# Kernel tuning notes

Measured on AMD Instinct MI355X. Metric: run time of the kernel, lower is better.

## Reference

```python
import jax, jax.numpy as jnp
import numpy as np
from jax import lax

B, T, I, H, L = 512, 2048, 16, 40, 3

def setup_inputs() -> dict:
    key = jax.random.key(0)
    ks = jax.random.split(key, 4 * L + 3)
    bound = 1.0 / np.sqrt(H)
    u = lambda k, shp: jax.random.uniform(k, shp, jnp.float32, -bound, bound)
    inp = {"x": jax.random.normal(ks[0], (B, T, I), jnp.float32)}
    for l in range(L):
        in_dim = I if l == 0 else H
        inp[f"w_ih{l}"] = u(ks[1 + 4 * l], (H, in_dim))
        inp[f"w_hh{l}"] = u(ks[2 + 4 * l], (H, H))
        inp[f"b_ih{l}"] = u(ks[3 + 4 * l], (H,))
        inp[f"b_hh{l}"] = u(ks[4 + 4 * l], (H,))
    inp["fc_w"] = u(ks[4 * L + 1], (1, H))
    inp["fc_b"] = u(ks[4 * L + 2], (1,))
    return inp

def _rnn_layer(x_seq, w_ih, w_hh, b_ih, b_hh):
    # Precompute input projection as one big GEMM: [B, T, H]
    xp = jnp.einsum('bti,hi->bth', x_seq, w_ih) + b_ih + b_hh
    h0 = jnp.zeros((x_seq.shape[0], w_hh.shape[0]), x_seq.dtype)
    def step(h, xt):  # xt: [B, H]
        h = jnp.tanh(xt + h @ w_hh.T)
        return h, h
    _, ys = lax.scan(step, h0, jnp.swapaxes(xp, 0, 1))  # [T, B, H]
    return jnp.swapaxes(ys, 0, 1)  # [B, T, H]

def reference(x, w_ih0, w_hh0, b_ih0, b_hh0,
              w_ih1, w_hh1, b_ih1, b_hh1,
              w_ih2, w_hh2, b_ih2, b_hh2, fc_w, fc_b):
    # Multi-layer tanh RNN (eval mode: inter-layer and final dropout are identity)
    h = _rnn_layer(x, w_ih0, w_hh0, b_ih0, b_hh0)
    h = _rnn_layer(h, w_ih1, w_hh1, b_ih1, b_hh1)
    h = _rnn_layer(h, w_ih2, w_hh2, b_ih2, b_hh2)
    last = h[:, -1, :]                     # [B, H]
    out = last @ fc_w.T + fc_b             # [B, 1]
    return out[:, 0]                       # [B]
```

## Files before the change

kernel.cpp:

```cpp
#include <hip/hip_runtime.h>
#include <cstddef>
#include <cstdint>

#define B_ 512
#define T_ 2048
#define I_ 16
#define H_ 40

typedef __fp16 half_t;
typedef half_t h2 __attribute__((ext_vector_type(2)));
typedef float f4 __attribute__((ext_vector_type(4)));

__device__ __forceinline__ float fast_tanh(float x) {
  float e = __builtin_amdgcn_exp2f(x * 2.8853900817779268f);
  return 1.0f - 2.0f * __builtin_amdgcn_rcpf(e + 1.0f);
}

__device__ __forceinline__ float dot2(h2 a, h2 b, float c) {
  return __builtin_amdgcn_fdot2(a, b, c, false);
}

__device__ __forceinline__ h2 cvtpk_v(float lo, float hi) {
  h2 r;
  asm volatile("v_cvt_pkrtz_f16_f32 %0, %1, %2" : "=v"(r) : "v"(lo), "v"(hi));
  return r;
}

#define PIN(v) asm volatile("" : "+v"(v))

#define GLOAD16(R0, R1, R2, R3, P)                                  \
  asm volatile("global_load_dwordx4 %0, %4, off\n\t"                \
               "global_load_dwordx4 %1, %4, off offset:16\n\t"      \
               "global_load_dwordx4 %2, %4, off offset:32\n\t"      \
               "global_load_dwordx4 %3, %4, off offset:48"          \
               : "=&v"(R0), "=&v"(R1), "=&v"(R2), "=&v"(R3)         \
               : "v"(P))

#define WAITX(N)                                                    \
  do {                                                              \
    asm volatile("s_waitcnt vmcnt(" #N ")" ::: "memory");           \
    __builtin_amdgcn_sched_barrier(0);                              \
  } while (0)

#define LOADW(DST, SRC, STR, N2)                                    \
  _Pragma("unroll") for (int k = 0; k < (N2); ++k) {                \
    DST[k][0] = (half_t)SRC[jr * (STR) + 2 * k];                    \
    DST[k][1] = (half_t)SRC[jr * (STR) + 2 * k + 1];                \
    PIN(DST[k]);                                                    \
  }

#define BCAST(NH, PAIRS) do {                                       \
  int nb_ = __builtin_amdgcn_update_dpp(                            \
      0, __builtin_bit_cast(int, (NH)), 0xB1, 0xf, 0xf, false);     \
  h2 pk_ = __builtin_amdgcn_cvt_pkrtz((NH),                         \
      __builtin_bit_cast(float, nb_));                              \
  int pkb_ = __builtin_bit_cast(int, pk_);                          \
  _Pragma("unroll") for (int p = 0; p < H_ / 2; ++p)                \
    PAIRS[p] = __builtin_bit_cast(h2,                               \
        __builtin_amdgcn_readlane(pkb_, 2 * p));                    \
} while (0)

#define HDS(PAIRS, W, A0, A1, A2, A3)                               \
  _Pragma("unroll") for (int p = 0; p < 5; ++p) {                   \
    A0 = dot2(PAIRS[4 * p + 0], (W)[4 * p + 0], A0);                \
    A1 = dot2(PAIRS[4 * p + 1], (W)[4 * p + 1], A1);                \
    A2 = dot2(PAIRS[4 * p + 2], (W)[4 * p + 2], A2);                \
    A3 = dot2(PAIRS[4 * p + 3], (W)[4 * p + 3], A3);                \
  }

#define STEP(XH) do {                                               \
                                             \
  float a0 = bias0, a1 = 0.f, a2 = 0.f, a3 = 0.f;                   \
  a0 = dot2(XH[0], w0i[0], a0); a1 = dot2(XH[1], w0i[1], a1);       \
  a2 = dot2(XH[2], w0i[2], a2); a3 = dot2(XH[3], w0i[3], a3);       \
  a0 = dot2(XH[4], w0i[4], a0); a1 = dot2(XH[5], w0i[5], a1);       \
  a2 = dot2(XH[6], w0i[6], a2); a3 = dot2(XH[7], w0i[7], a3);       \
  HDS(hp0, w0h, a0, a1, a2, a3);                        \
  const float nh0 = fast_tanh((a0 + a1) + (a2 + a3));               \
  BCAST(nh0, hp0);                                                  \
                                             \
  float b0 = bias1, b1 = 0.f, b2 = 0.f, b3 = 0.f;                   \
  HDS(hp0, w1i, b0, b1, b2, b3);                        \
  HDS(hp1, w1h, b0, b1, b2, b3);                        \
  const float nh1 = fast_tanh((b0 + b1) + (b2 + b3));               \
  BCAST(nh1, hp1);                                                  \
                                             \
  float c0 = bias2, c1 = 0.f, c2 = 0.f, c3 = 0.f;                   \
  HDS(hp1, w2i, c0, c1, c2, c3);                        \
  HDS(hp2, w2h, c0, c1, c2, c3);                        \
  nh2v = fast_tanh((c0 + c1) + (c2 + c3));                          \
  BCAST(nh2v, hp2);                                                 \
} while (0)

#define PACKX(XH, R0, R1, R2, R3)                                   \
  do {                                                              \
    XH[0] = cvtpk_v(R0[0], R0[1]); XH[1] = cvtpk_v(R0[2], R0[3]);   \
    XH[2] = cvtpk_v(R1[0], R1[1]); XH[3] = cvtpk_v(R1[2], R1[3]);   \
    XH[4] = cvtpk_v(R2[0], R2[1]); XH[5] = cvtpk_v(R2[2], R2[3]);   \
    XH[6] = cvtpk_v(R3[0], R3[1]); XH[7] = cvtpk_v(R3[2], R3[3]);   \
  } while (0)

__global__ __launch_bounds__(64)
__attribute__((amdgpu_waves_per_eu(1, 1)))
void rnn3_fused(const float* __restrict__ x,
                const float* __restrict__ wih0, const float* __restrict__ whh0,
                const float* __restrict__ bih0, const float* __restrict__ bhh0,
                const float* __restrict__ wih1, const float* __restrict__ whh1,
                const float* __restrict__ b_ih1, const float* __restrict__ bhh1,
                const float* __restrict__ wih2, const float* __restrict__ whh2,
                const float* __restrict__ bih2, const float* __restrict__ bhh2,
                const float* __restrict__ fcw, const float* __restrict__ fcb,
                float* __restrict__ out) {
  const int b = blockIdx.x;
  const int j = threadIdx.x;
  const int jr = (j < H_) ? j : (H_ - 1);

  h2 w0i[I_ / 2], w0h[H_ / 2], w1i[H_ / 2], w1h[H_ / 2], w2i[H_ / 2], w2h[H_ / 2];
  LOADW(w0i, wih0, I_, I_ / 2)
  LOADW(w0h, whh0, H_, H_ / 2)
  LOADW(w1i, wih1, H_, H_ / 2)
  LOADW(w1h, whh1, H_, H_ / 2)
  LOADW(w2i, wih2, H_, H_ / 2)
  LOADW(w2h, whh2, H_, H_ / 2)

  float bias0 = bih0[jr] + bhh0[jr];  PIN(bias0);
  float bias1 = b_ih1[jr] + bhh1[jr]; PIN(bias1);
  float bias2 = bih2[jr] + bhh2[jr];  PIN(bias2);

  h2 hp0[H_ / 2], hp1[H_ / 2], hp2[H_ / 2];
#pragma unroll
  for (int p = 0; p < H_ / 2; ++p) {
    hp0[p] = h2{(half_t)0.f, (half_t)0.f};
    hp1[p] = h2{(half_t)0.f, (half_t)0.f};
    hp2[p] = h2{(half_t)0.f, (half_t)0.f};
  }

  const float* __restrict__ xb = x + (size_t)b * (T_ * I_);

  f4 rA0, rA1, rA2, rA3, rB0, rB1, rB2, rB3;
  GLOAD16(rA0, rA1, rA2, rA3, xb + 0 * I_);
  GLOAD16(rB0, rB1, rB2, rB3, xb + 1 * I_);

  float nh2v = 0.f;
  h2 xh[8];

  for (int t = 0; t < T_; t += 2) {
    WAITX(4);
    PACKX(xh, rA0, rA1, rA2, rA3);
    STEP(xh);
    { const float* pf = xb + (size_t)((t + 2 < T_) ? t + 2 : T_ - 1) * I_;
      GLOAD16(rA0, rA1, rA2, rA3, pf); }
    WAITX(4);
    PACKX(xh, rB0, rB1, rB2, rB3);
    STEP(xh);
    { const float* pf = xb + (size_t)((t + 3 < T_) ? t + 3 : T_ - 1) * I_;
      GLOAD16(rB0, rB1, rB2, rB3, pf); }
  }

  asm volatile("s_waitcnt vmcnt(0)" ::: "memory");
  __builtin_amdgcn_sched_barrier(0);
  PIN(rA0); PIN(rA1); PIN(rA2); PIN(rA3);
  PIN(rB0); PIN(rB1); PIN(rB2); PIN(rB3);

  const float fw = (j < H_) ? fcw[j] : 0.f;
  float v = nh2v * fw;
#pragma unroll
  for (int off = 32; off > 0; off >>= 1) v += __shfl_down(v, off);
  if (j == 0) out[b] = v + fcb[0];
}

extern "C" void kernel_launch(void* const* d_in, const int* in_sizes, int n_in,
                              void* d_out, int out_size, void* d_ws, size_t ws_size,
                              hipStream_t stream) {
  (void)in_sizes; (void)n_in; (void)d_ws; (void)ws_size; (void)out_size;
  const float* x    = (const float*)d_in[0];
  const float* wih0 = (const float*)d_in[1];
  const float* whh0 = (const float*)d_in[2];
  const float* bih0 = (const float*)d_in[3];
  const float* bhh0 = (const float*)d_in[4];
  const float* wih1 = (const float*)d_in[5];
  const float* whh1 = (const float*)d_in[6];
  const float* bih1 = (const float*)d_in[7];
  const float* bhh1 = (const float*)d_in[8];
  const float* wih2 = (const float*)d_in[9];
  const float* whh2 = (const float*)d_in[10];
  const float* bih2 = (const float*)d_in[11];
  const float* bhh2 = (const float*)d_in[12];
  const float* fcw  = (const float*)d_in[13];
  const float* fcb  = (const float*)d_in[14];
  float* out = (float*)d_out;

  hipLaunchKernelGGL(rnn3_fused, dim3(B_), dim3(64), 0, stream,
                     x, wih0, whh0, bih0, bhh0,
                     wih1, whh1, bih1, bhh1,
                     wih2, whh2, bih2, bhh2,
                     fcw, fcb, out);
}
```

Measured before the change: 926.3 us.

## Replace packed fp16 dot2 with scalar FMAs, bpermute broadcast, plain x loads

The packed v_dot2 fp16 accumulations become pairs of scalar fp32 FMAs on converted halves, and the x input skips fp16 packing and is multiplied in fp32. The hidden-state broadcast now uses ds_bpermute in place of readlane. The hand-written inline-asm global loads with explicit vmcnt waits are replaced by ordinary vector loads, leaving scheduling to the compiler. Together these roughly double the VALU instruction count per step and put LDS-path latency on the serial recurrence, and without explicit waits the prefetch overlap may be lost.

```diff
diff --git a/kernel.cpp b/kernel.cpp
--- a/kernel.cpp
+++ b/kernel.cpp
@@ -16,31 +16,14 @@
   return 1.0f - 2.0f * __builtin_amdgcn_rcpf(e + 1.0f);
 }
 
-__device__ __forceinline__ float dot2(h2 a, h2 b, float c) {
-  return __builtin_amdgcn_fdot2(a, b, c, false);
+__device__ __forceinline__ float fmx(half_t a, half_t b, float c) {
+  return __builtin_fmaf((float)a, (float)b, c);
 }
-
-__device__ __forceinline__ h2 cvtpk_v(float lo, float hi) {
-  h2 r;
-  asm volatile("v_cvt_pkrtz_f16_f32 %0, %1, %2" : "=v"(r) : "v"(lo), "v"(hi));
-  return r;
+__device__ __forceinline__ float fmxf(float a, half_t b, float c) {
+  return __builtin_fmaf(a, (float)b, c);
 }
 
 #define PIN(v) asm volatile("" : "+v"(v))
-
-#define GLOAD16(R0, R1, R2, R3, P)                                  \
-  asm volatile("global_load_dwordx4 %0, %4, off\n\t"                \
-               "global_load_dwordx4 %1, %4, off offset:16\n\t"      \
-               "global_load_dwordx4 %2, %4, off offset:32\n\t"      \
-               "global_load_dwordx4 %3, %4, off offset:48"          \
-               : "=&v"(R0), "=&v"(R1), "=&v"(R2), "=&v"(R3)         \
-               : "v"(P))
-
-#define WAITX(N)                                                    \
-  do {                                                              \
-    asm volatile("s_waitcnt vmcnt(" #N ")" ::: "memory");           \
-    __builtin_amdgcn_sched_barrier(0);                              \
-  } while (0)
 
 #define LOADW(DST, SRC, STR, N2)                                    \
   _Pragma("unroll") for (int k = 0; k < (N2); ++k) {                \
@@ -57,34 +40,51 @@
   int pkb_ = __builtin_bit_cast(int, pk_);                          \
   _Pragma("unroll") for (int p = 0; p < H_ / 2; ++p)                \
     PAIRS[p] = __builtin_bit_cast(h2,                               \
-        __builtin_amdgcn_readlane(pkb_, 2 * p));                    \
+        __builtin_amdgcn_ds_bpermute(8 * p, pkb_));                 \
 } while (0)
 
 #define HDS(PAIRS, W, A0, A1, A2, A3)                               \
   _Pragma("unroll") for (int p = 0; p < 5; ++p) {                   \
-    A0 = dot2(PAIRS[4 * p + 0], (W)[4 * p + 0], A0);                \
-    A1 = dot2(PAIRS[4 * p + 1], (W)[4 * p + 1], A1);                \
-    A2 = dot2(PAIRS[4 * p + 2], (W)[4 * p + 2], A2);                \
-    A3 = dot2(PAIRS[4 * p + 3], (W)[4 * p + 3], A3);                \
+    A0 = fmx(PAIRS[4 * p + 0][0], (W)[4 * p + 0][0], A0);           \
+    A1 = fmx(PAIRS[4 * p + 1][0], (W)[4 * p + 1][0], A1);           \
+    A2 = fmx(PAIRS[4 * p + 2][0], (W)[4 * p + 2][0], A2);           \
+    A3 = fmx(PAIRS[4 * p + 3][0], (W)[4 * p + 3][0], A3);           \
+    A0 = fmx(PAIRS[4 * p + 0][1], (W)[4 * p + 0][1], A0);           \
+    A1 = fmx(PAIRS[4 * p + 1][1], (W)[4 * p + 1][1], A1);           \
+    A2 = fmx(PAIRS[4 * p + 2][1], (W)[4 * p + 2][1], A2);           \
+    A3 = fmx(PAIRS[4 * p + 3][1], (W)[4 * p + 3][1], A3);           \
   }
 
-#define STEP(XH) do {                                               \
-                                             \
+#define XDOT(R0, R1, R2, R3, A0, A1, A2, A3) do {                   \
+  A0 = fmxf(R0[0], w0i[0][0], A0);                                  \
+  A1 = fmxf(R0[1], w0i[0][1], A1);                                  \
+  A2 = fmxf(R0[2], w0i[1][0], A2);                                  \
+  A3 = fmxf(R0[3], w0i[1][1], A3);                                  \
+  A0 = fmxf(R1[0], w0i[2][0], A0);                                  \
+  A1 = fmxf(R1[1], w0i[2][1], A1);                                  \
+  A2 = fmxf(R1[2], w0i[3][0], A2);                                  \
+  A3 = fmxf(R1[3], w0i[3][1], A3);                                  \
+  A0 = fmxf(R2[0], w0i[4][0], A0);                                  \
+  A1 = fmxf(R2[1], w0i[4][1], A1);                                  \
+  A2 = fmxf(R2[2], w0i[5][0], A2);                                  \
+  A3 = fmxf(R2[3], w0i[5][1], A3);                                  \
+  A0 = fmxf(R3[0], w0i[6][0], A0);                                  \
+  A1 = fmxf(R3[1], w0i[6][1], A1);                                  \
+  A2 = fmxf(R3[2], w0i[7][0], A2);                                  \
+  A3 = fmxf(R3[3], w0i[7][1], A3);                                  \
+} while (0)
+
+#define STEP(R0, R1, R2, R3) do {                                   \
   float a0 = bias0, a1 = 0.f, a2 = 0.f, a3 = 0.f;                   \
-  a0 = dot2(XH[0], w0i[0], a0); a1 = dot2(XH[1], w0i[1], a1);       \
-  a2 = dot2(XH[2], w0i[2], a2); a3 = dot2(XH[3], w0i[3], a3);       \
-  a0 = dot2(XH[4], w0i[4], a0); a1 = dot2(XH[5], w0i[5], a1);       \
-  a2 = dot2(XH[6], w0i[6], a2); a3 = dot2(XH[7], w0i[7], a3);       \
+  XDOT(R0, R1, R2, R3, a0, a1, a2, a3);                             \
   HDS(hp0, w0h, a0, a1, a2, a3);                        \
   const float nh0 = fast_tanh((a0 + a1) + (a2 + a3));               \
   BCAST(nh0, hp0);                                                  \
-                                             \
   float b0 = bias1, b1 = 0.f, b2 = 0.f, b3 = 0.f;                   \
   HDS(hp0, w1i, b0, b1, b2, b3);                        \
   HDS(hp1, w1h, b0, b1, b2, b3);                        \
   const float nh1 = fast_tanh((b0 + b1) + (b2 + b3));               \
   BCAST(nh1, hp1);                                                  \
-                                             \
   float c0 = bias2, c1 = 0.f, c2 = 0.f, c3 = 0.f;                   \
   HDS(hp1, w2i, c0, c1, c2, c3);                        \
   HDS(hp2, w2h, c0, c1, c2, c3);                        \
@@ -92,13 +92,10 @@
   BCAST(nh2v, hp2);                                                 \
 } while (0)
 
-#define PACKX(XH, R0, R1, R2, R3)                                   \
-  do {                                                              \
-    XH[0] = cvtpk_v(R0[0], R0[1]); XH[1] = cvtpk_v(R0[2], R0[3]);   \
-    XH[2] = cvtpk_v(R1[0], R1[1]); XH[3] = cvtpk_v(R1[2], R1[3]);   \
-    XH[4] = cvtpk_v(R2[0], R2[1]); XH[5] = cvtpk_v(R2[2], R2[3]);   \
-    XH[6] = cvtpk_v(R3[0], R3[1]); XH[7] = cvtpk_v(R3[2], R3[3]);   \
-  } while (0)
+#define LOADX4(R0, R1, R2, R3, P) do {                              \
+  const f4* q_ = (const f4*)(P);                                    \
+  R0 = q_[0]; R1 = q_[1]; R2 = q_[2]; R3 = q_[3];                   \
+} while (0)
 
 __global__ __launch_bounds__(64)
 __attribute__((amdgpu_waves_per_eu(1, 1)))
@@ -137,30 +134,20 @@
 
   const float* __restrict__ xb = x + (size_t)b * (T_ * I_);
 
-  f4 rA0, rA1, rA2, rA3, rB0, rB1, rB2, rB3;
-  GLOAD16(rA0, rA1, rA2, rA3, xb + 0 * I_);
-  GLOAD16(rB0, rB1, rB2, rB3, xb + 1 * I_);
+  f4 xA0, xA1, xA2, xA3, xB0, xB1, xB2, xB3;
+  LOADX4(xA0, xA1, xA2, xA3, xb);
+  LOADX4(xB0, xB1, xB2, xB3, xb + I_);
 
   float nh2v = 0.f;
-  h2 xh[8];
 
   for (int t = 0; t < T_; t += 2) {
-    WAITX(4);
-    PACKX(xh, rA0, rA1, rA2, rA3);
-    STEP(xh);
-    { const float* pf = xb + (size_t)((t + 2 < T_) ? t + 2 : T_ - 1) * I_;
-      GLOAD16(rA0, rA1, rA2, rA3, pf); }
-    WAITX(4);
-    PACKX(xh, rB0, rB1, rB2, rB3);
-    STEP(xh);
-    { const float* pf = xb + (size_t)((t + 3 < T_) ? t + 3 : T_ - 1) * I_;
-      GLOAD16(rB0, rB1, rB2, rB3, pf); }
+    STEP(xA0, xA1, xA2, xA3);
+    { const int tf = (t + 2 < T_) ? t + 2 : T_ - 1;
+      LOADX4(xA0, xA1, xA2, xA3, xb + (size_t)tf * I_); }
+    STEP(xB0, xB1, xB2, xB3);
+    { const int tf = (t + 3 < T_) ? t + 3 : T_ - 1;
+      LOADX4(xB0, xB1, xB2, xB3, xb + (size_t)tf * I_); }
   }
-
-  asm volatile("s_waitcnt vmcnt(0)" ::: "memory");
-  __builtin_amdgcn_sched_barrier(0);
-  PIN(rA0); PIN(rA1); PIN(rA2); PIN(rA3);
-  PIN(rB0); PIN(rB1); PIN(rB2); PIN(rB3);
 
   const float fw = (j < H_) ? fcw[j] : 0.f;
   float v = nh2v * fw;
```

Result: slower. 1.686 ms (+82.0%).
